# Optimization experiments

Measured on AMD Instinct MI355X. Metric: run time of the kernel, lower is better.

## Reference

```python
import jax, jax.numpy as jnp
import numpy as np

B, S, D, H = 2, 2048, 1024, 16
HD = D // H  # head_dim = 64


def setup_inputs() -> dict:
    key = jax.random.key(0)
    ks = jax.random.split(key, 9)
    sc = 1.0 / np.sqrt(D)
    return {
        "X": jax.random.normal(ks[0], (B, S, D), jnp.float32),
        "Wq": jax.random.normal(ks[1], (D, D), jnp.float32) * sc,
        "bq": jnp.zeros((D,), jnp.float32),
        "Wk": jax.random.normal(ks[2], (D, D), jnp.float32) * sc,
        "bk": jnp.zeros((D,), jnp.float32),
        "Wv": jax.random.normal(ks[3], (D, D), jnp.float32) * sc,
        "bv": jnp.zeros((D,), jnp.float32),
        "Wo": jax.random.normal(ks[4], (D, D), jnp.float32) * sc,
        "bo": jnp.zeros((D,), jnp.float32),
    }


def reference(X, Wq, bq, Wk, bk, Wv, bv, Wo, bo):
    b, s, d = X.shape
    q = (X @ Wq + bq).reshape(b, s, H, HD).transpose(0, 2, 1, 3)  # [B,H,S,HD]
    k = (X @ Wk + bk).reshape(b, s, H, HD).transpose(0, 2, 1, 3)
    v = (X @ Wv + bv).reshape(b, s, H, HD).transpose(0, 2, 1, 3)
    score = jnp.einsum("bhqd,bhkd->bhqk", q, k) / jnp.sqrt(jnp.float32(HD))
    causal = jnp.tril(jnp.ones((s, s), bool))  # [S,S]
    score = jnp.where(causal[None, None], score, -jnp.inf)
    attn = jax.nn.softmax(score, axis=-1)
    out = jnp.einsum("bhqk,bhkd->bhqd", attn, v)  # [B,H,S,HD]
    out = out.transpose(0, 2, 1, 3).reshape(b, s, d)
    return out @ Wo + bo
```

## Files before the change

kernel.cpp:

```cpp
#include <hip/hip_runtime.h>
#include <hip/hip_bf16.h>
#include <math.h>

#define B_SZ 2
#define S_SZ 2048
#define D_SZ 1024
#define H_SZ 16
#define HD_SZ 64
constexpr int M_ROWS = B_SZ * S_SZ;

typedef __bf16 bf16x8 __attribute__((ext_vector_type(8)));
typedef __bf16 bf16x4 __attribute__((ext_vector_type(4)));
typedef float f32x4 __attribute__((ext_vector_type(4)));

#define GLOAD_LDS16(gsrc, ldst)                                              \
  __builtin_amdgcn_global_load_lds(                                          \
      (const __attribute__((address_space(1))) void*)(gsrc),                 \
      (__attribute__((address_space(3))) void*)(ldst), 16, 0, 0)

__global__ __launch_bounds__(256) void cvt_bf16(const float* __restrict__ in,
                                                __bf16* __restrict__ out,
                                                int n8) {
  const int i = blockIdx.x * 256 + threadIdx.x;
  if (i >= n8) return;
  const float4 a = *reinterpret_cast<const float4*>(&in[i * 8]);
  const float4 b = *reinterpret_cast<const float4*>(&in[i * 8 + 4]);
  bf16x8 o;
  o[0] = (__bf16)a.x; o[1] = (__bf16)a.y; o[2] = (__bf16)a.z; o[3] = (__bf16)a.w;
  o[4] = (__bf16)b.x; o[5] = (__bf16)b.y; o[6] = (__bf16)b.z; o[7] = (__bf16)b.w;
  *reinterpret_cast<bf16x8*>(&out[i * 8]) = o;
}

__global__ __launch_bounds__(256) void cvt_w_t_all(const float* __restrict__ W0,
                                                   const float* __restrict__ W1,
                                                   const float* __restrict__ W2,
                                                   const float* __restrict__ W3,
                                                   __bf16* __restrict__ Wt) {
  __shared__ float Ts[32][33];
  const int z = blockIdx.z;
  const float* W = z == 0 ? W0 : (z == 1 ? W1 : (z == 2 ? W2 : W3));
  __bf16* out = Wt + (size_t)z * 1024 * 1024;
  const int k0 = blockIdx.x * 32, n0 = blockIdx.y * 32;
  const int tr = threadIdx.x >> 3;
  const int tc = (threadIdx.x & 7) * 4;
  const float4 v = *reinterpret_cast<const float4*>(&W[(size_t)(k0 + tr) * 1024 + n0 + tc]);
  Ts[tr][tc + 0] = v.x;
  Ts[tr][tc + 1] = v.y;
  Ts[tr][tc + 2] = v.z;
  Ts[tr][tc + 3] = v.w;
  __syncthreads();
  bf16x4 o;
#pragma unroll
  for (int j = 0; j < 4; ++j) o[j] = (__bf16)Ts[tc + j][tr];
  *reinterpret_cast<bf16x4*>(&out[(size_t)(n0 + tr) * 1024 + k0 + tc]) = o;
}

__global__ __launch_bounds__(256) void transpose_v(const __bf16* __restrict__ V,
                                                   __bf16* __restrict__ Vt) {
  constexpr int TST = 66;
  __shared__ __bf16 T[64 * TST];
  const int bh = blockIdx.y;
  const int s0 = blockIdx.x * 64;
  const size_t base = (size_t)bh * S_SZ * HD_SZ;
  const int tid = threadIdx.x;
  for (int i = tid; i < 512; i += 256) {
    const int r = i >> 3, c = (i & 7) * 8;
    *reinterpret_cast<bf16x8*>(&T[r * TST + c]) =
        *reinterpret_cast<const bf16x8*>(&V[base + (size_t)(s0 + r) * 64 + c]);
  }
  __syncthreads();
  const size_t obase = (size_t)bh * HD_SZ * S_SZ;
  for (int i = tid; i < 512; i += 256) {
    const int d = i >> 3, c = (i & 7) * 8;
    bf16x8 o;
#pragma unroll
    for (int j = 0; j < 8; ++j) o[j] = T[(c + j) * TST + d];
    *reinterpret_cast<bf16x8*>(&Vt[obase + (size_t)d * S_SZ + s0 + c]) = o;
  }
}

template <int MODE>
__global__ __launch_bounds__(256) void gemm_mfma(
    const __bf16* __restrict__ Ab, const __bf16* __restrict__ Bt,
    const float* __restrict__ bias0, const float* __restrict__ bias1,
    const float* __restrict__ bias2, float* __restrict__ C0,
    __bf16* __restrict__ Q0, __bf16* __restrict__ K0, __bf16* __restrict__ V0,
    int M, int N, int K) {
  __shared__ __bf16 As[128 * 32];
  __shared__ __bf16 Bs[128 * 32];

  const int tid = threadIdx.x;
  const int lane = tid & 63;
  const int w = tid >> 6;
  const int lr = lane & 15, lg = lane >> 4;
  const int wr = w >> 1, wc = w & 1;
  const int bm = blockIdx.x * 128;
  const int bn = blockIdx.y * 128;

  const int r0 = tid >> 2, c0 = (tid & 3) * 8;
  const int r1 = (tid + 256) >> 2, c1 = ((tid + 256) & 3) * 8;
  const __bf16* aS0 = &Ab[(size_t)(bm + r0) * K + c0];
  const __bf16* aS1 = &Ab[(size_t)(bm + r1) * K + c1];
  const __bf16* bS0 = &Bt[(size_t)(bn + r0) * K + c0];
  const __bf16* bS1 = &Bt[(size_t)(bn + r1) * K + c1];
  __bf16* aD0 = &As[w * 512];
  __bf16* aD1 = &As[2048 + w * 512];
  __bf16* bD0 = &Bs[w * 512];
  __bf16* bD1 = &Bs[2048 + w * 512];

  f32x4 acc[4][4] = {};

  for (int k0 = 0; k0 < K; k0 += 32) {
    if (k0) __syncthreads();
    GLOAD_LDS16(aS0, aD0);
    GLOAD_LDS16(aS1, aD1);
    GLOAD_LDS16(bS0, bD0);
    GLOAD_LDS16(bS1, bD1);
    aS0 += 32; aS1 += 32; bS0 += 32; bS1 += 32;
    __syncthreads();

    bf16x8 af[4], bfr[4];
#pragma unroll
    for (int i = 0; i < 4; ++i)
      af[i] = *reinterpret_cast<const bf16x8*>(&As[(wr * 64 + i * 16 + lr) * 32 + lg * 8]);
#pragma unroll
    for (int j = 0; j < 4; ++j)
      bfr[j] = *reinterpret_cast<const bf16x8*>(&Bs[(wc * 64 + j * 16 + lr) * 32 + lg * 8]);
#pragma unroll
    for (int i = 0; i < 4; ++i)
#pragma unroll
      for (int j = 0; j < 4; ++j)
        acc[i][j] = __builtin_amdgcn_mfma_f32_16x16x32_bf16(af[i], bfr[j], acc[i][j], 0, 0, 0);
  }

  if (MODE == 0) {
#pragma unroll
    for (int j = 0; j < 4; ++j) {
      const int n = bn + wc * 64 + j * 16 + lr;
      const float bs = bias0[n];
#pragma unroll
      for (int i = 0; i < 4; ++i) {
        const int mrow = bm + wr * 64 + i * 16 + lg * 4;
#pragma unroll
        for (int r = 0; r < 4; ++r)
          C0[(size_t)(mrow + r) * N + n] = acc[i][j][r] + bs;
      }
    }
  } else {
    const int which = bn >> 10;
    __bf16* dst = which == 0 ? Q0 : (which == 1 ? K0 : V0);
    const float* bp = which == 0 ? bias0 : (which == 1 ? bias1 : bias2);
    const float scale = which == 0 ? 0.18033688011112042f : 1.0f;
#pragma unroll
    for (int j = 0; j < 4; ++j) {
      const int nn = (bn & 1023) + wc * 64 + j * 16 + lr;
      const int hh = nn >> 6, hd = nn & 63;
      const float bs = bp[nn];
#pragma unroll
      for (int i = 0; i < 4; ++i) {
        const int mrow = bm + wr * 64 + i * 16 + lg * 4;
#pragma unroll
        for (int r = 0; r < 4; ++r) {
          const int m = mrow + r;
          const int bb = m >> 11, ss = m & (S_SZ - 1);
          dst[(((size_t)(bb * H_SZ + hh)) * S_SZ + ss) * HD_SZ + hd] =
              (__bf16)((acc[i][j][r] + bs) * scale);
        }
      }
    }
  }
}

__global__ __launch_bounds__(256) void attn_mfma(const __bf16* __restrict__ Q,
                                                 const __bf16* __restrict__ Kg,
                                                 const __bf16* __restrict__ Vtg,
                                                 __bf16* __restrict__ Aout) {
  constexpr int PST = 76;
  __shared__ __bf16 Ks[2][64 * 64];
  __shared__ __bf16 Vts[2][64 * 64];
  __shared__ __bf16 Ps[4][16 * PST];

  const int tid = threadIdx.x;
  const int lane = tid & 63;
  const int w = tid >> 6;
  const int lr = lane & 15;
  const int lg = lane >> 4;

  const int flat = blockIdx.x;
  const int qb = 31 - (flat >> 5);
  const int hb = flat & 31;
  const int h = hb >> 1, b = hb & 1;
  const size_t base = (size_t)(b * H_SZ + h) * S_SZ * HD_SZ;
  const int q0 = qb * 64 + w * 16;

  bf16x8 aq[2];
#pragma unroll
  for (int hh = 0; hh < 2; ++hh)
    aq[hh] = *reinterpret_cast<const bf16x8*>(
        &Q[base + (size_t)(q0 + lr) * 64 + hh * 32 + lg * 8]);

  const int srow = lane >> 3;
  const int schunk = (lane & 7) ^ (srow & 7);

  bf16x8 ones8;
#pragma unroll
  for (int j = 0; j < 8; ++j) ones8[j] = (__bf16)1.0f;

  f32x4 oacc[4] = {};
  f32x4 oacc_l = {};

  const int ntiles = qb + 1;

  const int rbA = w * 16, rbB = w * 16 + 8;
  const __bf16* kS0 = &Kg[base + (size_t)(rbA + srow) * 64 + schunk * 8];
  const __bf16* kS1 = &Kg[base + (size_t)(rbB + srow) * 64 + schunk * 8];
  const __bf16* vS0 = &Vtg[base + (size_t)(rbA + srow) * S_SZ + schunk * 8];
  const __bf16* vS1 = &Vtg[base + (size_t)(rbB + srow) * S_SZ + schunk * 8];

  auto ISSUE = [&](int buf) {
    GLOAD_LDS16(kS0, &Ks[buf][rbA * 64]);
    GLOAD_LDS16(kS1, &Ks[buf][rbB * 64]);
    GLOAD_LDS16(vS0, &Vts[buf][rbA * 64]);
    GLOAD_LDS16(vS1, &Vts[buf][rbB * 64]);
  };

  ISSUE(0);
  __syncthreads();
  int cur = 0;

  for (int t0 = 0; t0 < ntiles; ++t0) {
    if (t0 + 1 < ntiles) {
      kS0 += 64 * 64; kS1 += 64 * 64;
      vS0 += 64;      vS1 += 64;
      ISSUE(cur ^ 1);
    }

    f32x4 s[4];
    __builtin_amdgcn_s_setprio(1);
#pragma unroll
    for (int t = 0; t < 4; ++t) {
      const int row = t * 16 + lr;
      const bf16x8 k0f = *reinterpret_cast<const bf16x8*>(
          &Ks[cur][row * 64 + ((lg ^ (lr & 7)) * 8)]);
      const bf16x8 k1f = *reinterpret_cast<const bf16x8*>(
          &Ks[cur][row * 64 + (((4 | lg) ^ (lr & 7)) * 8)]);
      f32x4 z = (f32x4){0.f, 0.f, 0.f, 0.f};
      z = __builtin_amdgcn_mfma_f32_16x16x32_bf16(aq[0], k0f, z, 0, 0, 0);
      z = __builtin_amdgcn_mfma_f32_16x16x32_bf16(aq[1], k1f, z, 0, 0, 0);
      s[t] = z;
    }
    __builtin_amdgcn_s_setprio(0);

    if (t0 == qb) {
#pragma unroll
      for (int t = 0; t < 4; ++t) {
        const int key = t0 * 64 + t * 16 + lr;
#pragma unroll
        for (int r = 0; r < 4; ++r) {
          const int qrow = q0 + lg * 4 + r;
          if (key > qrow) s[t][r] = -INFINITY;
        }
      }
    }

#pragma unroll
    for (int t = 0; t < 4; ++t)
#pragma unroll
      for (int r = 0; r < 4; ++r)
        Ps[w][(lg * 4 + r) * PST + t * 16 + lr] =
            (__bf16)__builtin_amdgcn_exp2f(s[t][r]);
    asm volatile("s_waitcnt lgkmcnt(0)" ::: "memory");
    __builtin_amdgcn_sched_barrier(0);

    __builtin_amdgcn_s_setprio(1);
#pragma unroll
    for (int kh = 0; kh < 2; ++kh) {
      const bf16x8 pa = *reinterpret_cast<const bf16x8*>(
          &Ps[w][lr * PST + kh * 32 + lg * 8]);
#pragma unroll
      for (int dc = 0; dc < 4; ++dc) {
        const int row = dc * 16 + lr;
        const bf16x8 vf = *reinterpret_cast<const bf16x8*>(
            &Vts[cur][row * 64 + (((kh * 4 + lg) ^ (lr & 7)) * 8)]);
        oacc[dc] = __builtin_amdgcn_mfma_f32_16x16x32_bf16(pa, vf, oacc[dc], 0, 0, 0);
      }
      oacc_l = __builtin_amdgcn_mfma_f32_16x16x32_bf16(pa, ones8, oacc_l, 0, 0, 0);
    }
    __builtin_amdgcn_s_setprio(0);

    __syncthreads();
    cur ^= 1;
  }

#pragma unroll
  for (int r = 0; r < 4; ++r) {
    const float inv = 1.f / oacc_l[r];
    const int qg = q0 + lg * 4 + r;
#pragma unroll
    for (int dc = 0; dc < 4; ++dc)
      Aout[(size_t)(b * S_SZ + qg) * D_SZ + h * 64 + dc * 16 + lr] =
          (__bf16)(oacc[dc][r] * inv);
  }
}

extern "C" void kernel_launch(void* const* d_in, const int* in_sizes, int n_in,
                              void* d_out, int out_size, void* d_ws,
                              size_t ws_size, hipStream_t stream) {
  const float* X = (const float*)d_in[0];
  const float* Wq = (const float*)d_in[1];
  const float* bq = (const float*)d_in[2];
  const float* Wk = (const float*)d_in[3];
  const float* bk = (const float*)d_in[4];
  const float* Wv = (const float*)d_in[5];
  const float* bv = (const float*)d_in[6];
  const float* Wo = (const float*)d_in[7];
  const float* bo = (const float*)d_in[8];
  float* out = (float*)d_out;

  const size_t elems = (size_t)M_ROWS * D_SZ;
  const size_t welems = (size_t)D_SZ * D_SZ;
  __bf16* Xb = (__bf16*)d_ws;
  __bf16* Wt = Xb + elems;
  __bf16* Q = Wt + 4 * welems;
  __bf16* K = Q + elems;
  __bf16* V = K + elems;
  __bf16* Vt = V + elems;
  __bf16* Ahb = Vt + elems;

  cvt_bf16<<<(int)(elems / 8 / 256), 256, 0, stream>>>(X, Xb, (int)(elems / 8));
  cvt_w_t_all<<<dim3(32, 32, 4), 256, 0, stream>>>(Wq, Wk, Wv, Wo, Wt);

  gemm_mfma<1><<<dim3(M_ROWS / 128, 3072 / 128), 256, 0, stream>>>(
      Xb, Wt, bq, bk, bv, nullptr, Q, K, V, M_ROWS, 3072, D_SZ);

  transpose_v<<<dim3(32, 32), 256, 0, stream>>>(V, Vt);

  attn_mfma<<<dim3(1024), 256, 0, stream>>>(Q, K, Vt, Ahb);

  gemm_mfma<0><<<dim3(M_ROWS / 128, D_SZ / 128), 256, 0, stream>>>(
      Ahb, Wt + 3 * welems, bo, nullptr, nullptr, out, nullptr, nullptr,
      nullptr, M_ROWS, D_SZ, D_SZ);
}
```

Before: 114.5 us.

## Double-buffer GEMM LDS tiles and use partial vmcnt waits in attention

The projection GEMM gets two LDS buffers so the next K-slice's global-to-LDS loads are issued before computing the current one. Full syncthreads drains are replaced by s_waitcnt vmcnt(4) plus a raw barrier in both the GEMM and attention kernels. The prefetch can then stay in flight across the barrier instead of being waited on. In attention, the P tile staging buffer is shrunk to 16x32 halves written per kh step, cutting LDS footprint, at the cost of an extra lgkm wait per half. The hand-placed waitcnt values rely on exactly four outstanding loads per stage.

New measurement: 116.0 us. About the same (+1.3%).

```diff
diff --git a/kernel.cpp b/kernel.cpp
--- a/kernel.cpp
+++ b/kernel.cpp
@@ -86,8 +86,8 @@
     const float* __restrict__ bias2, float* __restrict__ C0,
     __bf16* __restrict__ Q0, __bf16* __restrict__ K0, __bf16* __restrict__ V0,
     int M, int N, int K) {
-  __shared__ __bf16 As[128 * 32];
-  __shared__ __bf16 Bs[128 * 32];
+  __shared__ __bf16 As[2][128 * 32];
+  __shared__ __bf16 Bs[2][128 * 32];
 
   const int tid = threadIdx.x;
   const int lane = tid & 63;
@@ -103,34 +103,52 @@
   const __bf16* aS1 = &Ab[(size_t)(bm + r1) * K + c1];
   const __bf16* bS0 = &Bt[(size_t)(bn + r0) * K + c0];
   const __bf16* bS1 = &Bt[(size_t)(bn + r1) * K + c1];
-  __bf16* aD0 = &As[w * 512];
-  __bf16* aD1 = &As[2048 + w * 512];
-  __bf16* bD0 = &Bs[w * 512];
-  __bf16* bD1 = &Bs[2048 + w * 512];
 
   f32x4 acc[4][4] = {};
 
+  auto STAGE = [&](int buf) {
+    GLOAD_LDS16(aS0, &As[buf][w * 512]);
+    GLOAD_LDS16(aS1, &As[buf][2048 + w * 512]);
+    GLOAD_LDS16(bS0, &Bs[buf][w * 512]);
+    GLOAD_LDS16(bS1, &Bs[buf][2048 + w * 512]);
+    aS0 += 32; aS1 += 32; bS0 += 32; bS1 += 32;
+  };
+
+  STAGE(0);
+  asm volatile("s_waitcnt vmcnt(0)" ::: "memory");
+  __builtin_amdgcn_s_barrier();
+  __builtin_amdgcn_sched_barrier(0);
+  int cur = 0;
+
   for (int k0 = 0; k0 < K; k0 += 32) {
-    if (k0) __syncthreads();
-    GLOAD_LDS16(aS0, aD0);
-    GLOAD_LDS16(aS1, aD1);
-    GLOAD_LDS16(bS0, bD0);
-    GLOAD_LDS16(bS1, bD1);
-    aS0 += 32; aS1 += 32; bS0 += 32; bS1 += 32;
-    __syncthreads();
+    const bool has_next = (k0 + 32 < K);
+    if (has_next) STAGE(cur ^ 1);
+    if (k0) {
+      if (has_next)
+        asm volatile("s_waitcnt vmcnt(4)" ::: "memory");
+      else
+        asm volatile("s_waitcnt vmcnt(0)" ::: "memory");
+      __builtin_amdgcn_s_barrier();
+      __builtin_amdgcn_sched_barrier(0);
+    }
 
     bf16x8 af[4], bfr[4];
 #pragma unroll
     for (int i = 0; i < 4; ++i)
-      af[i] = *reinterpret_cast<const bf16x8*>(&As[(wr * 64 + i * 16 + lr) * 32 + lg * 8]);
+      af[i] = *reinterpret_cast<const bf16x8*>(&As[cur][(wr * 64 + i * 16 + lr) * 32 + lg * 8]);
 #pragma unroll
     for (int j = 0; j < 4; ++j)
-      bfr[j] = *reinterpret_cast<const bf16x8*>(&Bs[(wc * 64 + j * 16 + lr) * 32 + lg * 8]);
+      bfr[j] = *reinterpret_cast<const bf16x8*>(&Bs[cur][(wc * 64 + j * 16 + lr) * 32 + lg * 8]);
+    __builtin_amdgcn_s_setprio(1);
 #pragma unroll
     for (int i = 0; i < 4; ++i)
 #pragma unroll
       for (int j = 0; j < 4; ++j)
         acc[i][j] = __builtin_amdgcn_mfma_f32_16x16x32_bf16(af[i], bfr[j], acc[i][j], 0, 0, 0);
+    __builtin_amdgcn_s_setprio(0);
+    __builtin_amdgcn_sched_barrier(0);
+    __builtin_amdgcn_s_barrier();
+    cur ^= 1;
   }
 
   if (MODE == 0) {
@@ -175,7 +193,7 @@
                                                  const __bf16* __restrict__ Kg,
                                                  const __bf16* __restrict__ Vtg,
                                                  __bf16* __restrict__ Aout) {
-  constexpr int PST = 76;
+  constexpr int PST = 40;
   __shared__ __bf16 Ks[2][64 * 64];
   __shared__ __bf16 Vts[2][64 * 64];
   __shared__ __bf16 Ps[4][16 * PST];
@@ -200,7 +218,7 @@
         &Q[base + (size_t)(q0 + lr) * 64 + hh * 32 + lg * 8]);
 
   const int srow = lane >> 3;
-  const int schunk = (lane & 7) ^ (srow & 7);
+  const int schunk = (lane & 7) ^ srow;
 
   bf16x8 ones8;
 #pragma unroll
@@ -225,14 +243,25 @@
   };
 
   ISSUE(0);
-  __syncthreads();
+  asm volatile("s_waitcnt vmcnt(0)" ::: "memory");
+  __builtin_amdgcn_s_barrier();
+  __builtin_amdgcn_sched_barrier(0);
   int cur = 0;
 
   for (int t0 = 0; t0 < ntiles; ++t0) {
-    if (t0 + 1 < ntiles) {
+    const bool has_next = (t0 + 1 < ntiles);
+    if (has_next) {
       kS0 += 64 * 64; kS1 += 64 * 64;
       vS0 += 64;      vS1 += 64;
       ISSUE(cur ^ 1);
+    }
+    if (t0) {
+      if (has_next)
+        asm volatile("s_waitcnt vmcnt(4)" ::: "memory");
+      else
+        asm volatile("s_waitcnt vmcnt(0)" ::: "memory");
+      __builtin_amdgcn_s_barrier();
+      __builtin_amdgcn_sched_barrier(0);
     }
 
     f32x4 s[4];
@@ -267,16 +296,20 @@
     for (int t = 0; t < 4; ++t)
 #pragma unroll
       for (int r = 0; r < 4; ++r)
-        Ps[w][(lg * 4 + r) * PST + t * 16 + lr] =
-            (__bf16)__builtin_amdgcn_exp2f(s[t][r]);
-    asm volatile("s_waitcnt lgkmcnt(0)" ::: "memory");
-    __builtin_amdgcn_sched_barrier(0);
-
-    __builtin_amdgcn_s_setprio(1);
+        s[t][r] = __builtin_amdgcn_exp2f(s[t][r]);
+
+    __bf16* const psw = &Ps[w][0];
 #pragma unroll
     for (int kh = 0; kh < 2; ++kh) {
-      const bf16x8 pa = *reinterpret_cast<const bf16x8*>(
-          &Ps[w][lr * PST + kh * 32 + lg * 8]);
+#pragma unroll
+      for (int t2 = 0; t2 < 2; ++t2)
+#pragma unroll
+        for (int r = 0; r < 4; ++r)
+          psw[(lg * 4 + r) * PST + t2 * 16 + lr] = (__bf16)s[kh * 2 + t2][r];
+      asm volatile("s_waitcnt lgkmcnt(0)" ::: "memory");
+      __builtin_amdgcn_sched_barrier(0);
+      const bf16x8 pa = *reinterpret_cast<const bf16x8*>(&psw[lr * PST + lg * 8]);
+      __builtin_amdgcn_s_setprio(1);
 #pragma unroll
       for (int dc = 0; dc < 4; ++dc) {
         const int row = dc * 16 + lr;
@@ -285,10 +318,12 @@
         oacc[dc] = __builtin_amdgcn_mfma_f32_16x16x32_bf16(pa, vf, oacc[dc], 0, 0, 0);
       }
       oacc_l = __builtin_amdgcn_mfma_f32_16x16x32_bf16(pa, ones8, oacc_l, 0, 0, 0);
-    }
-    __builtin_amdgcn_s_setprio(0);
-
-    __syncthreads();
+      __builtin_amdgcn_s_setprio(0);
+      __builtin_amdgcn_sched_barrier(0);
+    }
+
+    __builtin_amdgcn_sched_barrier(0);
+    __builtin_amdgcn_s_barrier();
     cur ^= 1;
   }
 
```
